# Kernel tuning notes

Measured on AMD Instinct MI355X. Metric: run time of the kernel, lower is better.

Reference implementation:

```python
import math
import jax, jax.numpy as jnp
import numpy as np

B, S, D = 4, 2048, 512
H = 8
HD = D // H  # 64


def setup_inputs() -> dict:
    key = jax.random.key(0)
    k1, k2, k3, k4, k5 = jax.random.split(key, 5)
    x = jax.random.normal(k1, (B, S, D), dtype=jnp.float32)
    # additive causal mask, broadcast over [H, B, S, S] in the original code
    neg_inf = jnp.float32(-1e9)
    mask = jnp.where(jnp.tril(jnp.ones((S, S), dtype=bool)), 0.0, neg_inf).astype(jnp.float32)
    Wqkv = jax.random.normal(k2, (D, 3 * D), dtype=jnp.float32) * (1.0 / math.sqrt(D))
    bqkv = jax.random.normal(k3, (3 * D,), dtype=jnp.float32) * 0.02
    Wo = jax.random.normal(k4, (D, D), dtype=jnp.float32) * (1.0 / math.sqrt(D))
    bo = jax.random.normal(k5, (D,), dtype=jnp.float32) * 0.02
    return {"x": x, "mask": mask, "Wqkv": Wqkv, "bqkv": bqkv, "Wo": Wo, "bo": bo}


def reference(x, mask, Wqkv, bqkv, Wo, bo):
    b, s, d = x.shape
    hd = d // H
    qkv = x @ Wqkv + bqkv                       # [b, s, 3d]
    # match torch: reshape to [b, s, H, 3*hd], move heads, chunk last dim
    qkv = qkv.reshape(b, s, H, 3 * hd).transpose(0, 2, 1, 3)  # [b, H, s, 3hd]
    q, k, v = jnp.split(qkv, 3, axis=-1)        # each [b, H, s, hd]
    scale = 1.0 / math.sqrt(hd)
    scores = jnp.einsum('bhqd,bhkd->bhqk', q, k) * scale
    scores = scores + mask                      # mask [s, s] broadcasts over [b, H, s, s]
    attn = jax.nn.softmax(scores, axis=-1)
    vals = jnp.einsum('bhqk,bhkd->bhqd', attn, v)
    vals = vals.transpose(0, 2, 1, 3).reshape(b, s, d)
    return vals @ Wo + bo
```

## Files before the change

### kernel.cpp

```cpp
#include <hip/hip_runtime.h>
#include <hip/hip_bf16.h>

#define S_ 2048
#define D_ 512
#define HD_ 64
#define HH_ 8
#define M_ 8192

typedef __attribute__((ext_vector_type(8))) short short8;
typedef __attribute__((ext_vector_type(4))) short short4v;
typedef __attribute__((ext_vector_type(4))) float f32x4;

__device__ __forceinline__ unsigned short f2bf(float f) {
  unsigned u = __builtin_bit_cast(unsigned, f);
  u += 0x7fffu + ((u >> 16) & 1u);
  return (unsigned short)(u >> 16);
}

__device__ __forceinline__ f32x4 mfma16(short8 a, short8 b, f32x4 c) {
  return __builtin_amdgcn_mfma_f32_16x16x32_bf16(a, b, c, 0, 0, 0);
}

#define GLOAD_LDS16(gp, lp)                                                        \
  __builtin_amdgcn_global_load_lds(                                                \
      (const __attribute__((address_space(1))) void*)(gp),                         \
      (__attribute__((address_space(3))) void*)(lp), 16, 0, 0)

__global__ __launch_bounds__(256) void k_cvt_all(const float* __restrict__ x,
                                                 short* __restrict__ xb,
                                                 const float* __restrict__ wqkv,
                                                 short* __restrict__ wqkvt,
                                                 const float* __restrict__ wo,
                                                 short* __restrict__ wot) {
  __shared__ short T[32][33];
  const int bid = blockIdx.x;
  if (bid < 2048) {
    int idx = bid * 256 + threadIdx.x;
    const float4* p = (const float4*)x;
    float4 a = p[idx * 2];
    float4 b = p[idx * 2 + 1];
    short8 v;
    v[0] = (short)f2bf(a.x); v[1] = (short)f2bf(a.y);
    v[2] = (short)f2bf(a.z); v[3] = (short)f2bf(a.w);
    v[4] = (short)f2bf(b.x); v[5] = (short)f2bf(b.y);
    v[6] = (short)f2bf(b.z); v[7] = (short)f2bf(b.w);
    int row = idx >> 6;
    int dst = row * 512 + ((idx >> 3) & 7) * 64 + (((idx & 7) ^ (row & 7)) << 3);
    *(short8*)&xb[dst] = v;
    return;
  }
  const float* w;
  short* wt;
  int C, bx, by;
  if (bid < 2816) {
    w = wqkv; wt = wqkvt; C = 1536;
    int b = bid - 2048; bx = b % 48; by = b / 48;
  } else {
    w = wo; wt = wot; C = 512;
    int b = bid - 2816; bx = b % 16; by = b / 16;
  }
  const int tx = threadIdx.x & 31, ty = threadIdx.x >> 5;
  const int n0 = bx * 32, k0 = by * 32;
#pragma unroll
  for (int i = 0; i < 4; i++) {
    int k = k0 + ty + 8 * i;
    T[ty + 8 * i][tx] = (short)f2bf(w[k * C + n0 + tx]);
  }
  __syncthreads();
#pragma unroll
  for (int i = 0; i < 4; i++) {
    int n = n0 + ty + 8 * i;
    int k = k0 + tx;
    int ksw = (k & ~63) | ((((k >> 3) & 7) ^ (n & 7)) << 3) | (k & 7);
    wt[n * 512 + ksw] = T[tx][ty + 8 * i];
  }
}

template <int MODE>
__global__ __launch_bounds__(256) void k_gemm(const short* __restrict__ A,
                                              const short* __restrict__ Bt,
                                              const float* __restrict__ bias,
                                              short* __restrict__ Qo,
                                              short* __restrict__ Ko,
                                              short* __restrict__ VTo,
                                              float* __restrict__ Fo) {
  __shared__ short As[2][8192];
  __shared__ short Bs[2][4096];
  const int tid = threadIdx.x;
  const int w = tid >> 6, l = tid & 63, g = l >> 4, c = l & 15;
  const int lid = blockIdx.x;
  const int lidp = (lid & 7) * 192 + (lid >> 3);
  const int bm = (lidp / 24) * 128, bn = (lidp % 24) * 64;
  const int wm = (w >> 1) * 64, wn = (w & 1) * 32;
  f32x4 acc[4][2] = {};
  const short* Ap = A + (bm + (l >> 3)) * 512 + (l & 7) * 8;
  const short* Bp = Bt + (bn + (l >> 3)) * 512 + (l & 7) * 8;
  const int sa0 = w * 4;
  const int sb0 = w * 2;

#define GSTAGE(buf, k0)                                                       \
  {                                                                           \
    GLOAD_LDS16(Ap + (sa0 + 0) * 4096 + (k0), &As[buf][(sa0 + 0) * 512]);     \
    GLOAD_LDS16(Ap + (sa0 + 1) * 4096 + (k0), &As[buf][(sa0 + 1) * 512]);     \
    GLOAD_LDS16(Ap + (sa0 + 2) * 4096 + (k0), &As[buf][(sa0 + 2) * 512]);     \
    GLOAD_LDS16(Ap + (sa0 + 3) * 4096 + (k0), &As[buf][(sa0 + 3) * 512]);     \
    GLOAD_LDS16(Bp + (sb0 + 0) * 4096 + (k0), &Bs[buf][(sb0 + 0) * 512]);     \
    GLOAD_LDS16(Bp + (sb0 + 1) * 4096 + (k0), &Bs[buf][(sb0 + 1) * 512]);     \
  }

  GSTAGE(0, 0);
  __syncthreads();

  const int cs = c & 7;
  int cur = 0;
  for (int k0 = 0; k0 < 512; k0 += 64) {
    if (k0 + 64 < 512) GSTAGE(cur ^ 1, k0 + 64);

    short8 a0[4], a1[4], b0[2], b1[2];
#pragma unroll
    for (int mt = 0; mt < 4; mt++) {
      const short* r = &As[cur][(wm + mt * 16 + c) * 64];
      a0[mt] = *(const short8*)&r[(g ^ cs) << 3];
      a1[mt] = *(const short8*)&r[((g + 4) ^ cs) << 3];
    }
#pragma unroll
    for (int nt = 0; nt < 2; nt++) {
      const short* r = &Bs[cur][(wn + nt * 16 + c) * 64];
      b0[nt] = *(const short8*)&r[(g ^ cs) << 3];
      b1[nt] = *(const short8*)&r[((g + 4) ^ cs) << 3];
    }
#pragma unroll
    for (int mt = 0; mt < 4; mt++)
#pragma unroll
      for (int nt = 0; nt < 2; nt++) {
        acc[mt][nt] = mfma16(a0[mt], b0[nt], acc[mt][nt]);
        acc[mt][nt] = mfma16(a1[mt], b1[nt], acc[mt][nt]);
      }

    __syncthreads();
    cur ^= 1;
  }
#undef GSTAGE

  if (MODE == 0) {
    const float QS = 0.125f * 1.4426950408889634f;
#pragma unroll
    for (int nt = 0; nt < 2; nt++) {
      int n = bn + wn + nt * 16 + c;
      float bv = bias[n];
      int h = n / 192;
      int t = n - h * 192;
      int type = t >> 6;
      int hd = t & 63;
      float sc = (type == 0) ? QS : 1.0f;
#pragma unroll
      for (int mt = 0; mt < 4; mt++) {
        int m0 = bm + wm + mt * 16 + 4 * g;
        int b = m0 >> 11, ss = m0 & 2047;
        int bh = b * 8 + h;
        if (type == 2) {
          int sw = (ss & ~63) | (((((ss >> 3) & 7) ^ (hd & 7)) << 3)) | (ss & 7);
          short4v pk;
#pragma unroll
          for (int r = 0; r < 4; r++) pk[r] = (short)f2bf(acc[mt][nt][r] + bv);
          *(short4v*)&VTo[(bh * 64 + hd) * 2048 + sw] = pk;
        } else if (type == 1) {
#pragma unroll
          for (int r = 0; r < 4; r++) {
            int s = ss + r;
            int hds = ((((hd >> 3) ^ (s & 7)) << 3)) | (hd & 7);
            Ko[(bh * 2048 + s) * 64 + hds] = (short)f2bf(acc[mt][nt][r] + bv);
          }
        } else {
#pragma unroll
          for (int r = 0; r < 4; r++)
            Qo[(bh * 2048 + ss + r) * 64 + hd] = (short)f2bf((acc[mt][nt][r] + bv) * sc);
        }
      }
    }
  } else {
#pragma unroll
    for (int nt = 0; nt < 2; nt++) {
      int n = bn + wn + nt * 16 + c;
      float bv = bias[n];
#pragma unroll
      for (int mt = 0; mt < 4; mt++) {
        int m0 = bm + wm + mt * 16 + 4 * g;
#pragma unroll
        for (int r = 0; r < 4; r++) Fo[(m0 + r) * 512 + n] = acc[mt][nt][r] + bv;
      }
    }
  }
}

__global__ __launch_bounds__(256) void k_gemm2(const short* __restrict__ A,
                                               const short* __restrict__ Bt,
                                               const float* __restrict__ bias,
                                               float* __restrict__ Fo) {
  __shared__ short As[2][4096];
  __shared__ short Bs[2][4096];
  const int tid = threadIdx.x;
  const int w = tid >> 6, l = tid & 63, g = l >> 4, c = l & 15;
  const int lid = blockIdx.x;
  const int lidp = (lid & 7) * 128 + (lid >> 3);
  const int bm = (lidp >> 3) * 64, bn = (lidp & 7) * 64;
  const int wm = (w >> 1) * 32, wn = (w & 1) * 32;
  f32x4 acc[2][2] = {};
  const short* Ap = A + (bm + (l >> 3)) * 512 + (l & 7) * 8;
  const short* Bp = Bt + (bn + (l >> 3)) * 512 + (l & 7) * 8;
  const int s0 = w * 2;

#define G2STAGE(buf, k0)                                                      \
  {                                                                           \
    GLOAD_LDS16(Ap + (s0 + 0) * 4096 + (k0), &As[buf][(s0 + 0) * 512]);       \
    GLOAD_LDS16(Ap + (s0 + 1) * 4096 + (k0), &As[buf][(s0 + 1) * 512]);       \
    GLOAD_LDS16(Bp + (s0 + 0) * 4096 + (k0), &Bs[buf][(s0 + 0) * 512]);       \
    GLOAD_LDS16(Bp + (s0 + 1) * 4096 + (k0), &Bs[buf][(s0 + 1) * 512]);       \
  }

  G2STAGE(0, 0);
  __syncthreads();

  const int cs = c & 7;
  int cur = 0;
  for (int k0 = 0; k0 < 512; k0 += 64) {
    if (k0 + 64 < 512) G2STAGE(cur ^ 1, k0 + 64);

    short8 a0[2], a1[2], b0[2], b1[2];
#pragma unroll
    for (int mt = 0; mt < 2; mt++) {
      const short* r = &As[cur][(wm + mt * 16 + c) * 64];
      a0[mt] = *(const short8*)&r[(g ^ cs) << 3];
      a1[mt] = *(const short8*)&r[((g + 4) ^ cs) << 3];
    }
#pragma unroll
    for (int nt = 0; nt < 2; nt++) {
      const short* r = &Bs[cur][(wn + nt * 16 + c) * 64];
      b0[nt] = *(const short8*)&r[(g ^ cs) << 3];
      b1[nt] = *(const short8*)&r[((g + 4) ^ cs) << 3];
    }
#pragma unroll
    for (int mt = 0; mt < 2; mt++)
#pragma unroll
      for (int nt = 0; nt < 2; nt++) {
        acc[mt][nt] = mfma16(a0[mt], b0[nt], acc[mt][nt]);
        acc[mt][nt] = mfma16(a1[mt], b1[nt], acc[mt][nt]);
      }

    __syncthreads();
    cur ^= 1;
  }
#undef G2STAGE

#pragma unroll
  for (int nt = 0; nt < 2; nt++) {
    int n = bn + wn + nt * 16 + c;
    float bv = bias[n];
#pragma unroll
    for (int mt = 0; mt < 2; mt++) {
      int m0 = bm + wm + mt * 16 + 4 * g;
#pragma unroll
      for (int r = 0; r < 4; r++) Fo[(m0 + r) * 512 + n] = acc[mt][nt][r] + bv;
    }
  }
}

__global__ __launch_bounds__(512, 6) void k_attn(const short* __restrict__ Q,
                                                 const short* __restrict__ K,
                                                 const short* __restrict__ VT,
                                                 short* __restrict__ ctx) {
  __shared__ short KVs[2][8192];
  __shared__ short P[8][1024];
  const int tid = threadIdx.x;
  const int w = tid >> 6, l = tid & 63, g = l >> 4, c = l & 15;
  const int rg = w & 3, pp = w >> 2;

  const int x = blockIdx.x;
  const int bh = x & 31;
  const int j = 31 - (x >> 5);
  const int qbase = j * 64 + rg * 16;
  const int nss = j + 1;

  const short* Qb = Q + bh * S_ * HD_;
  const short* Kb = K + bh * S_ * HD_;
  const short* Vb = VT + bh * HD_ * S_;

  const int kr = tid >> 3, kc8 = (tid & 7) * 8;

#define STAGE(buf, kv0)                                                      \
  {                                                                          \
    GLOAD_LDS16(Kb + ((kv0) + kr) * 64 + kc8, &KVs[buf][w * 512]);           \
    GLOAD_LDS16(Vb + kr * 2048 + (kv0) + kc8, &KVs[buf][4096 + w * 512]);    \
  }

  short* Pw = &P[w][0];
  const int bb = bh >> 3, hh = bh & 7;
  const f32x4 CINIT = {-16.f, -16.f, -16.f, -16.f};

  short8 qf0 = *(const short8*)&Qb[(qbase + c) * 64 + 8 * g];
  short8 qf1 = *(const short8*)&Qb[(qbase + c) * 64 + 8 * g + 32];

  f32x4 o[4];
  float psum[4];
#pragma unroll
  for (int nt = 0; nt < 4; nt++) o[nt] = f32x4{0.f, 0.f, 0.f, 0.f};
#pragma unroll
  for (int r = 0; r < 4; r++) psum[r] = 0.f;

  STAGE(0, 0);
  __syncthreads();

  int cur = 0;
  for (int t = 0; t < nss; ++t) {
    if (t + 1 < nss) STAGE(cur ^ 1, (t + 1) * 64);

    const short* Kt = &KVs[cur][pp * 2048];
    const short* Vt = &KVs[cur][4096];
    const int kv0 = t * 64 + pp * 32;

    f32x4 sa[2];
#pragma unroll
    for (int nt = 0; nt < 2; nt++) {
      const short* r = &Kt[(nt * 16 + c) * 64];
      short8 kf0 = *(const short8*)&r[(g ^ (c & 7)) << 3];
      short8 kf1 = *(const short8*)&r[((g + 4) ^ (c & 7)) << 3];
      sa[nt] = mfma16(qf0, kf0, CINIT);
      sa[nt] = mfma16(qf1, kf1, sa[nt]);
    }

    if (kv0 + 32 > qbase) {
#pragma unroll
      for (int nt = 0; nt < 2; nt++) {
        int kv = kv0 + nt * 16 + c;
#pragma unroll
        for (int r = 0; r < 4; r++) {
          int qrow = qbase + 4 * g + r;
          if (kv > qrow) sa[nt][r] = -1e30f;
        }
      }
    }

#pragma unroll
    for (int nt = 0; nt < 2; nt++)
#pragma unroll
      for (int r = 0; r < 4; r++) {
        float pv = __builtin_amdgcn_exp2f(sa[nt][r]);
        psum[r] += pv;
        int row = 4 * g + r;
        int col = nt * 16 + c;
        int off = (row << 6) + ((((col >> 3) ^ (row & 7)) << 3)) + (col & 7);
        Pw[off] = (short)(__builtin_bit_cast(unsigned, pv) >> 16);
      }

    short8 pa = *(const short8*)&Pw[(c << 6) + ((g ^ (c & 7)) << 3)];
#pragma unroll
    for (int nt = 0; nt < 4; nt++) {
      short8 vb = *(const short8*)&Vt[((nt * 16 + c) << 6) +
                                      (((4 * pp + g) ^ (c & 7)) << 3)];
      o[nt] = mfma16(pa, vb, o[nt]);
    }

    __syncthreads();
    cur ^= 1;
  }

#pragma unroll
  for (int off = 1; off < 16; off <<= 1)
#pragma unroll
    for (int r = 0; r < 4; r++) psum[r] += __shfl_xor(psum[r], off, 64);

  float* scr = (float*)&KVs[0][0];
  float* pscr = (float*)&P[0][0];
  if (pp == 1) {
#pragma unroll
    for (int nt = 0; nt < 4; nt++)
#pragma unroll
      for (int r = 0; r < 4; r++)
        scr[rg * 1088 + (4 * g + r) * 68 + nt * 16 + c] = o[nt][r];
    if (c == 0) {
#pragma unroll
      for (int r = 0; r < 4; r++) pscr[rg * 16 + 4 * g + r] = psum[r];
    }
  }
  __syncthreads();
  if (pp == 0) {
    float inv[4];
#pragma unroll
    for (int r = 0; r < 4; r++)
      inv[r] = 1.0f / (psum[r] + pscr[rg * 16 + 4 * g + r]);
#pragma unroll
    for (int nt = 0; nt < 4; nt++)
#pragma unroll
      for (int r = 0; r < 4; r++) {
        float ov = o[nt][r] + scr[rg * 1088 + (4 * g + r) * 68 + nt * 16 + c];
        int srow = qbase + 4 * g + r;
        int colsw = hh * 64 + (((nt * 2 + (c >> 3)) ^ (srow & 7)) << 3) + (c & 7);
        ctx[(bb * S_ + srow) * 512 + colsw] = (short)f2bf(ov * inv[r]);
      }
  }
#undef STAGE
}


extern "C" void kernel_launch(void* const* d_in, const int* in_sizes, int n_in,
                              void* d_out, int out_size, void* d_ws, size_t ws_size,
                              hipStream_t stream) {
  const float* x = (const float*)d_in[0];
  const float* Wqkv = (const float*)d_in[2];
  const float* bqkv = (const float*)d_in[3];
  const float* Wo = (const float*)d_in[4];
  const float* bo = (const float*)d_in[5];
  float* out = (float*)d_out;

  char* ws = (char*)d_ws;
  short* xb    = (short*)(ws + 0);
  short* wqkvt = (short*)(ws + 8388608);
  short* wot   = (short*)(ws + 9961472);
  short* Qw    = (short*)(ws + 10485760);
  short* Kw    = (short*)(ws + 18874368);
  short* VTw   = (short*)(ws + 27262976);
  short* ctx   = (short*)(ws + 35651584);

  k_cvt_all<<<3072, 256, 0, stream>>>(x, xb, Wqkv, wqkvt, Wo, wot);

  k_gemm<0><<<1536, 256, 0, stream>>>(xb, wqkvt, bqkv, Qw, Kw, VTw, nullptr);

  k_attn<<<1024, 512, 0, stream>>>(Qw, Kw, VTw, ctx);

  k_gemm2<<<1024, 256, 0, stream>>>(ctx, wot, bo, out);
}
```

Baseline: 76.72 us.

## Load V fragments directly from global and reorder causal query-block schedule

```diff
diff --git a/kernel.cpp b/kernel.cpp
--- a/kernel.cpp
+++ b/kernel.cpp
@@ -265,19 +265,20 @@
   }
 }
 
-__global__ __launch_bounds__(512, 6) void k_attn(const short* __restrict__ Q,
+__global__ __launch_bounds__(512, 8) void k_attn(const short* __restrict__ Q,
                                                  const short* __restrict__ K,
                                                  const short* __restrict__ VT,
                                                  short* __restrict__ ctx) {
-  __shared__ short KVs[2][8192];
-  __shared__ short P[8][1024];
+  __shared__ short SMEM[16384];
   const int tid = threadIdx.x;
   const int w = tid >> 6, l = tid & 63, g = l >> 4, c = l & 15;
   const int rg = w & 3, pp = w >> 2;
 
   const int x = blockIdx.x;
   const int bh = x & 31;
-  const int j = 31 - (x >> 5);
+  const int t5 = x >> 5;
+  const int qq = t5 >> 3, sq = t5 & 7;
+  const int j = (qq == 0) ? sq : (qq == 1) ? 15 - sq : (qq == 2) ? 16 + sq : 31 - sq;
   const int qbase = j * 64 + rg * 16;
   const int nss = j + 1;
 
@@ -285,20 +286,20 @@
   const short* Kb = K + bh * S_ * HD_;
   const short* Vb = VT + bh * HD_ * S_;
 
-  const int kr = tid >> 3, kc8 = (tid & 7) * 8;
-
 #define STAGE(buf, kv0)                                                      \
-  {                                                                          \
-    GLOAD_LDS16(Kb + ((kv0) + kr) * 64 + kc8, &KVs[buf][w * 512]);           \
-    GLOAD_LDS16(Vb + kr * 2048 + (kv0) + kc8, &KVs[buf][4096 + w * 512]);    \
-  }
-
-  short* Pw = &P[w][0];
+  GLOAD_LDS16(Kb + (kv0) * 64 + tid * 8, &SMEM[(buf) * 4096 + w * 512])
+
+  short* Pw = &SMEM[8192 + w * 1024];
   const int bb = bh >> 3, hh = bh & 7;
   const f32x4 CINIT = {-16.f, -16.f, -16.f, -16.f};
 
   short8 qf0 = *(const short8*)&Qb[(qbase + c) * 64 + 8 * g];
   short8 qf1 = *(const short8*)&Qb[(qbase + c) * 64 + 8 * g + 32];
+
+  const short* Vp[4];
+#pragma unroll
+  for (int nt = 0; nt < 4; nt++)
+    Vp[nt] = Vb + (nt * 16 + c) * 2048 + (((4 * pp + g) ^ (c & 7)) << 3);
 
   f32x4 o[4];
   float psum[4];
@@ -314,8 +315,7 @@
   for (int t = 0; t < nss; ++t) {
     if (t + 1 < nss) STAGE(cur ^ 1, (t + 1) * 64);
 
-    const short* Kt = &KVs[cur][pp * 2048];
-    const short* Vt = &KVs[cur][4096];
+    const short* Kt = &SMEM[cur * 4096 + pp * 2048];
     const int kv0 = t * 64 + pp * 32;
 
     f32x4 sa[2];
@@ -352,13 +352,17 @@
         Pw[off] = (short)(__builtin_bit_cast(unsigned, pv) >> 16);
       }
 
+    const int tb = t * 64;
+    short8 vv0 = *(const short8*)(Vp[0] + tb);
+    short8 vv1 = *(const short8*)(Vp[1] + tb);
+    short8 vv2 = *(const short8*)(Vp[2] + tb);
+    short8 vv3 = *(const short8*)(Vp[3] + tb);
+
     short8 pa = *(const short8*)&Pw[(c << 6) + ((g ^ (c & 7)) << 3)];
-#pragma unroll
-    for (int nt = 0; nt < 4; nt++) {
-      short8 vb = *(const short8*)&Vt[((nt * 16 + c) << 6) +
-                                      (((4 * pp + g) ^ (c & 7)) << 3)];
-      o[nt] = mfma16(pa, vb, o[nt]);
-    }
+    o[0] = mfma16(pa, vv0, o[0]);
+    o[1] = mfma16(pa, vv1, o[1]);
+    o[2] = mfma16(pa, vv2, o[2]);
+    o[3] = mfma16(pa, vv3, o[3]);
 
     __syncthreads();
     cur ^= 1;
@@ -369,8 +373,8 @@
 #pragma unroll
     for (int r = 0; r < 4; r++) psum[r] += __shfl_xor(psum[r], off, 64);
 
-  float* scr = (float*)&KVs[0][0];
-  float* pscr = (float*)&P[0][0];
+  float* scr = (float*)&SMEM[0];
+  float* pscr = scr + 4352;
   if (pp == 1) {
 #pragma unroll
     for (int nt = 0; nt < 4; nt++)
```

After: 100.5 us. 1.31x slower.
